# Performance work log

Hardware: AMD Instinct MI355X
Metric: run time of the kernel (lower is better)

The kernel has to match this reference:

```python
import jax, jax.numpy as jnp
import numpy as np

B, T, D = 256, 256, 96   # batch, seq (== block_size), d_model
H, E = 6, 16             # n_head, d_head = d_model // n_head
DFF = 4 * D              # feedforward hidden = 384
NOISE_STD = 0.1
EPS = 1e-5               # torch LayerNorm default eps


def setup_inputs() -> dict:
    key = jax.random.key(0)
    ks = jax.random.split(key, 10)
    s = 0.02
    return {
        "x":     jax.random.normal(ks[0], (B, T, D), jnp.float32),
        # per-head Q/K/V projections stacked: [H, D, E] (no bias, as in Head)
        "Wq":    jax.random.normal(ks[1], (H, D, E), jnp.float32) * s,
        "Wk":    jax.random.normal(ks[2], (H, D, E), jnp.float32) * s,
        "Wv":    jax.random.normal(ks[3], (H, D, E), jnp.float32) * s,
        "Wp":    jax.random.normal(ks[4], (D, D), jnp.float32) * s,
        "bp":    jnp.zeros((D,), jnp.float32),
        "ln1_g": jnp.ones((D,), jnp.float32),
        "ln1_b": jnp.zeros((D,), jnp.float32),
        "ln2_g": jnp.ones((D,), jnp.float32),
        "ln2_b": jnp.zeros((D,), jnp.float32),
        "W1":    jax.random.normal(ks[5], (D, DFF), jnp.float32) * s,
        "b1":    jnp.zeros((DFF,), jnp.float32),
        "W2":    jax.random.normal(ks[6], (DFF, D), jnp.float32) * s,
        "b2":    jnp.zeros((D,), jnp.float32),
    }


def layernorm(x, g, b):
    m = jnp.mean(x, axis=-1, keepdims=True)
    v = jnp.var(x, axis=-1, keepdims=True)
    return (x - m) * jax.lax.rsqrt(v + EPS) * g + b


def reference(x, Wq, Wk, Wv, Wp, bp, ln1_g, ln1_b, ln2_g, ln2_b, W1, b1, W2, b2):
    Bx, Tx, Dx = x.shape
    nk1, nk2 = jax.random.split(jax.random.key(42), 2)

    # --- self-attention branch (pre-norm) ---
    h = layernorm(x, ln1_g, ln1_b)
    q = jnp.einsum('btd,hde->bhte', h, Wq)
    k = jnp.einsum('btd,hde->bhte', h, Wk)
    v = jnp.einsum('btd,hde->bhte', h, Wv)
    scores = jnp.einsum('bhte,bhse->bhts', q, k) * (E ** -0.5)
    causal = jnp.tril(jnp.ones((Tx, Tx), bool))
    scores = jnp.where(causal, scores, -jnp.inf)
    a = jax.nn.softmax(scores, axis=-1)      # dropout = identity (eval)
    o = jnp.einsum('bhts,bhse->bhte', a, v)
    o = o.transpose(0, 2, 1, 3).reshape(Bx, Tx, Dx)  # concat heads
    o = o @ Wp + bp
    x = x + o + jax.random.normal(nk1, x.shape, x.dtype) * NOISE_STD

    # --- feedforward branch (pre-norm) ---
    h = layernorm(x, ln2_g, ln2_b)
    f = jax.nn.relu(h @ W1 + b1) @ W2 + b2   # dropout = identity (eval)
    x = x + f + jax.random.normal(nk2, x.shape, x.dtype) * NOISE_STD
    return x
```

## Files before the change

### kernel.cpp

```cpp
#include <hip/hip_runtime.h>
#include <hip/hip_bf16.h>
#include <stdint.h>


#define B_    256
#define T_    256
#define D_    96
#define H_    6
#define E_    16
#define DFF_  384
#define BT_   (B_*T_)
#define NTOK_ (BT_*D_)
#define WPN_  (96*96)
#define W1N_  (96*384)
#define W2N_  (384*96)
#define WTOT_ (WPN_+W1N_+W2N_)

typedef __hip_bfloat16 bf16;
typedef __attribute__((ext_vector_type(8))) short v8s;
typedef __attribute__((ext_vector_type(4))) float v4f;

__device__ __forceinline__ void wfence(){ __asm__ volatile("" ::: "memory"); }

__host__ __device__ inline uint32_t rotl32(uint32_t x, int r){ return (x<<r)|(x>>(32-r)); }

__host__ __device__ inline void tf2x32(uint32_t k0, uint32_t k1, uint32_t& x0, uint32_t& x1){
  uint32_t ks2 = k0 ^ k1 ^ 0x1BD11BDAu;
  x0 += k0; x1 += k1;
#define TF_R(r) { x0 += x1; x1 = rotl32(x1, r); x1 ^= x0; }
  TF_R(13) TF_R(15) TF_R(26) TF_R(6)
  x0 += k1;  x1 += ks2 + 1u;
  TF_R(17) TF_R(29) TF_R(16) TF_R(24)
  x0 += ks2; x1 += k0 + 2u;
  TF_R(13) TF_R(15) TF_R(26) TF_R(6)
  x0 += k0;  x1 += k1 + 3u;
  TF_R(17) TF_R(29) TF_R(16) TF_R(24)
  x0 += k1;  x1 += ks2 + 4u;
  TF_R(13) TF_R(15) TF_R(26) TF_R(6)
  x0 += ks2; x1 += k0 + 5u;
#undef TF_R
}

__device__ __forceinline__ float erfinv32(float x){
  float w = -0.69314718056f * __log2f((1.0f - x) * (1.0f + x));
  float p;
  if (w < 5.0f) {
    w -= 2.5f;
    p = 2.81022636e-08f;
    p = fmaf(p, w, 3.43273939e-07f);
    p = fmaf(p, w, -3.5233877e-06f);
    p = fmaf(p, w, -4.39150654e-06f);
    p = fmaf(p, w, 0.00021858087f);
    p = fmaf(p, w, -0.00125372503f);
    p = fmaf(p, w, -0.00417768164f);
    p = fmaf(p, w, 0.246640727f);
    p = fmaf(p, w, 1.50140941f);
  } else {
    w = sqrtf(w) - 3.0f;
    p = -0.000200214257f;
    p = fmaf(p, w, 0.000100950558f);
    p = fmaf(p, w, 0.00134934322f);
    p = fmaf(p, w, -0.00367342844f);
    p = fmaf(p, w, 0.00573950773f);
    p = fmaf(p, w, -0.0076224613f);
    p = fmaf(p, w, 0.00943887047f);
    p = fmaf(p, w, 1.00167406f);
    p = fmaf(p, w, 2.83297682f);
  }
  return p * x;
}

__device__ __forceinline__ float jax_normal(uint32_t k0, uint32_t k1, uint32_t j){
  uint32_t x0 = 0u, x1 = j;
  tf2x32(k0, k1, x0, x1);
  uint32_t bits = x0 ^ x1;
  float f = __uint_as_float((bits >> 9) | 0x3F800000u) - 1.0f;
  const float lo = -0.99999994f;
  float u = fmaxf(lo, fmaf(f, 2.0f, lo));
  return 1.41421356f * erfinv32(u);
}

__device__ __forceinline__ float blo(uint32_t u){ return __uint_as_float(u << 16); }
__device__ __forceinline__ float bhi(uint32_t u){ return __uint_as_float(u & 0xFFFF0000u); }
__device__ __forceinline__ uint16_t f2b(float f){
  union { bf16 h; uint16_t u; } x; x.h = __float2bfloat16(f); return x.u;
}
__device__ __forceinline__ uint32_t packbf(float a, float b){
  return (uint32_t)f2b(a) | ((uint32_t)f2b(b) << 16);
}

__global__ __launch_bounds__(256, 3)
void k_attn_fused(const float* __restrict__ x,
                  const float* __restrict__ Wq, const float* __restrict__ Wk,
                  const float* __restrict__ Wv,
                  const float* __restrict__ g1, const float* __restrict__ bln1,
                  bf16* __restrict__ o_ws,
                  const float* __restrict__ Wp, const float* __restrict__ W1,
                  const float* __restrict__ W2, bf16* __restrict__ wbuf)
{
  __shared__ __align__(16) uint16_t hts[64*104];
  __shared__ __align__(16) uint32_t wpl[48][52];
  __shared__ __align__(16) uint16_t Ks[256][24];
  __shared__ __align__(16) uint16_t Vt[16][264];

  const int tid  = threadIdx.x;
  const int bh   = blockIdx.x;
  const int b    = bh / H_, h = bh % H_;
  const int w    = tid >> 6;
  const int lane = tid & 63;
  const int quad = lane >> 4;
  const int l15  = lane & 15;

  if (tid < 54) {
    int id = bh*54 + tid;
    const float* src; bf16* dst; int k, n, N;
    if (id < WPN_)             { src = Wp; dst = wbuf;               k = id/96; n = id%96; N = 96; }
    else if (id < WPN_ + W1N_) { int t = id - WPN_;
                                 src = W1; dst = wbuf + WPN_;        k = t/384; n = t%384; N = 384; }
    else                       { int t = id - WPN_ - W1N_;
                                 src = W2; dst = wbuf + WPN_ + W1N_; k = t/96;  n = t%96;  N = 96; }
    int idx = ((k>>3)*(N>>4) + (n>>4))*128 + ((n&15)<<3) + (k&7);
    dst[idx] = __float2bfloat16(src[(size_t)k*N + n]);
  }

  for (int idx = tid; idx < 48*48; idx += 256) {
    int c = idx / 48, dp = idx % 48;
    int mat = c >> 4, e = c & 15;
    const float* Wm = (mat == 0 ? Wk : (mat == 1 ? Wv : Wq)) + h*(D_*E_);
    wpl[c][dp] = packbf(Wm[(2*dp)*16 + e], Wm[(2*dp+1)*16 + e]);
  }

  v4f qacc[4];
  {
    const int r  = lane >> 2;
    const int cg = lane & 3;
    float gv[24], bv[24];
    #pragma unroll
    for (int i = 0; i < 24; ++i) { gv[i] = g1[cg*24 + i]; bv[i] = bln1[cg*24 + i]; }

    for (int rt = 0; rt < 4; ++rt) {
      __syncthreads();
      const int lrow = w*16 + r;
      const int row  = rt*64 + lrow;
      const float4* xp = (const float4*)(x + ((size_t)(b*256 + row)*96 + cg*24));
      float xv[24];
      #pragma unroll
      for (int p = 0; p < 6; ++p) {
        float4 t4 = xp[p];
        xv[4*p+0] = t4.x; xv[4*p+1] = t4.y; xv[4*p+2] = t4.z; xv[4*p+3] = t4.w;
      }
      float s1 = 0.f, s2 = 0.f;
      #pragma unroll
      for (int i = 0; i < 24; ++i) { s1 += xv[i]; s2 = fmaf(xv[i], xv[i], s2); }
      s1 += __shfl_xor(s1, 1); s2 += __shfl_xor(s2, 1);
      s1 += __shfl_xor(s1, 2); s2 += __shfl_xor(s2, 2);
      float mm = s1 * (1.0f/96.0f);
      float rs = rsqrtf(s2 * (1.0f/96.0f) - mm*mm + 1e-5f);
      #pragma unroll
      for (int p = 0; p < 12; ++p) {
        float h0 = (xv[2*p]   - mm)*rs*gv[2*p]   + bv[2*p];
        float h1 = (xv[2*p+1] - mm)*rs*gv[2*p+1] + bv[2*p+1];
        *(uint32_t*)&hts[lrow*104 + cg*24 + 2*p] = packbf(h0, h1);
      }
      __syncthreads();

      v8s ah[3];
      #pragma unroll
      for (int ks = 0; ks < 3; ++ks)
        ah[ks] = *(const v8s*)&hts[(w*16 + l15)*104 + ks*32 + quad*8];
      #pragma unroll
      for (int nt = 0; nt < 3; ++nt) {
        v4f acc = {0.f,0.f,0.f,0.f};
        #pragma unroll
        for (int ks = 0; ks < 3; ++ks) {
          v8s bb = *(const v8s*)&wpl[nt*16 + l15][ks*16 + quad*4];
          acc = __builtin_amdgcn_mfma_f32_16x16x32_bf16(ah[ks], bb, acc, 0, 0, 0);
        }
        int tr0 = rt*64 + w*16 + quad*4;
        if (nt == 0) {
          #pragma unroll
          for (int r2 = 0; r2 < 4; ++r2) Ks[tr0 + r2][l15] = f2b(acc[r2]);
        } else if (nt == 1) {
          *(uint32_t*)&Vt[l15][tr0]     = packbf(acc[0], acc[1]);
          *(uint32_t*)&Vt[l15][tr0 + 2] = packbf(acc[2], acc[3]);
        } else {
          qacc[rt] = acc;
        }
      }
    }
  }
  __syncthreads();

  uint16_t* Pb = &hts[(w*16)*104];
  v8s qf[4];
  v8s zero8;
  #pragma unroll
  for (int j = 0; j < 8; ++j) zero8[j] = 0;
  #pragma unroll
  for (int rt = 0; rt < 4; ++rt) {
    wfence();
    #pragma unroll
    for (int r2 = 0; r2 < 4; ++r2)
      Pb[(quad*4 + r2)*40 + l15] = f2b(qacc[rt][r2] * 0.25f);
    wfence();
    qf[rt] = (quad < 2) ? *(const v8s*)&Pb[l15*40 + quad*8] : zero8;
  }

  v8s ones;
  #pragma unroll
  for (int j = 0; j < 8; ++j) ones[j] = (short)0x3F80;

  v4f oacc[4], lac[4];
  #pragma unroll
  for (int i = 0; i < 4; ++i) { oacc[i] = (v4f){0.f,0.f,0.f,0.f}; lac[i] = (v4f){0.f,0.f,0.f,0.f}; }

  for (int sb = 0; sb < 8; ++sb) {
    v8s kf0 = (quad < 2) ? *(const v8s*)&Ks[sb*32      + l15][quad*8] : zero8;
    v8s kf1 = (quad < 2) ? *(const v8s*)&Ks[sb*32 + 16 + l15][quad*8] : zero8;
    v8s vf  = *(const v8s*)&Vt[l15][sb*32 + quad*8];
    #pragma unroll
    for (int i = 0; i < 4; ++i) {
      int mt = 4*i + w;
      if (mt >= 2*sb) {
        v4f z = {0.f,0.f,0.f,0.f};
        v4f s0 = __builtin_amdgcn_mfma_f32_16x16x32_bf16(qf[i], kf0, z, 0, 0, 0);
        v4f s1 = __builtin_amdgcn_mfma_f32_16x16x32_bf16(qf[i], kf1, z, 0, 0, 0);
        const int qb  = mt*16 + quad*4;
        const int sc0 = sb*32 + l15, sc1 = sc0 + 16;
        wfence();
        #pragma unroll
        for (int r2 = 0; r2 < 4; ++r2) {
          float p0 = (sc0 > qb + r2) ? 0.f : __expf(s0[r2]);
          float p1 = (sc1 > qb + r2) ? 0.f : __expf(s1[r2]);
          Pb[(quad*4 + r2)*40 + l15]      = f2b(p0);
          Pb[(quad*4 + r2)*40 + 16 + l15] = f2b(p1);
        }
        wfence();
        v8s pf = *(const v8s*)&Pb[l15*40 + quad*8];
        oacc[i] = __builtin_amdgcn_mfma_f32_16x16x32_bf16(pf, vf,   oacc[i], 0, 0, 0);
        lac[i]  = __builtin_amdgcn_mfma_f32_16x16x32_bf16(pf, ones, lac[i],  0, 0, 0);
      }
    }
  }

  #pragma unroll
  for (int i = 0; i < 4; ++i) {
    int mt = 4*i + w;
    #pragma unroll
    for (int r2 = 0; r2 < 4; ++r2) {
      float inv = 1.0f / lac[i][r2];
      size_t idx = ((size_t)b*256 + mt*16 + quad*4 + r2)*96 + h*16 + l15;
      o_ws[idx] = __float2bfloat16(oacc[i][r2] * inv);
    }
  }
}

__global__ __launch_bounds__(256, 4)
void k_proj_ff(const float* __restrict__ x, const bf16* __restrict__ o_ws,
               const bf16* __restrict__ wb,
               const float* __restrict__ bp,
               const float* __restrict__ g2, const float* __restrict__ bln2,
               const float* __restrict__ b1, const float* __restrict__ b2,
               float* __restrict__ out,
               uint32_t n1k0, uint32_t n1k1, uint32_t n2k0, uint32_t n2k1)
{
  __shared__ __align__(16) uint16_t t2 [2][64][104];

  const bf16* wpb = wb;
  const bf16* w1b = wb + WPN_;
  const bf16* w2b = wb + WPN_ + W1N_;

  const int tid  = threadIdx.x;
  const int w    = tid >> 6;
  const int lane = tid & 63;
  const int quad = lane >> 4;
  const int l15  = lane & 15;
  const int rowbase = blockIdx.x * 64;
  const uint32_t jbase = (uint32_t)rowbase * 96u;

  #define BFRAG(Wb, Ndiv16, nt, k8) \
    (*(const v8s*)((Wb) + (((k8)*(Ndiv16) + (nt))*128 + l15*8)))

  float ff[24];
  {
    v8s ao[3];
    #pragma unroll
    for (int ks = 0; ks < 3; ++ks)
      ao[ks] = *(const v8s*)(o_ws + (size_t)(rowbase + w*16 + l15)*96 + ks*32 + quad*8);
    #pragma unroll
    for (int nt = 0; nt < 6; ++nt) {
      int col = nt*16 + l15;
      v4f acc = {0.f,0.f,0.f,0.f};
      #pragma unroll
      for (int ks = 0; ks < 3; ++ks)
        acc = __builtin_amdgcn_mfma_f32_16x16x32_bf16(ao[ks], BFRAG(wpb, 6, nt, ks*4+quad), acc, 0, 0, 0);
      float bpv = bp[col];
      #pragma unroll
      for (int r = 0; r < 4; ++r) {
        int row = w*16 + quad*4 + r;
        uint32_t j = jbase + (uint32_t)row*96u + (uint32_t)col;
        ff[nt*4+r] = acc[r] + bpv + x[j] + 0.1f * jax_normal(n1k0, n1k1, j);
      }
    }
  }

  {
    float mmv[4], rsv[4];
    #pragma unroll
    for (int r = 0; r < 4; ++r) {
      float s1 = 0.f, s2 = 0.f;
      #pragma unroll
      for (int nt = 0; nt < 6; ++nt) { float v = ff[nt*4+r]; s1 += v; s2 = fmaf(v, v, s2); }
      s1 += __shfl_xor(s1, 1); s2 += __shfl_xor(s2, 1);
      s1 += __shfl_xor(s1, 2); s2 += __shfl_xor(s2, 2);
      s1 += __shfl_xor(s1, 4); s2 += __shfl_xor(s2, 4);
      s1 += __shfl_xor(s1, 8); s2 += __shfl_xor(s2, 8);
      float mm = s1 * (1.0f/96.0f);
      mmv[r] = mm;
      rsv[r] = rsqrtf(s2 * (1.0f/96.0f) - mm*mm + 1e-5f);
    }
    float g2v[6], b2l[6];
    #pragma unroll
    for (int nt = 0; nt < 6; ++nt) { g2v[nt] = g2[nt*16 + l15]; b2l[nt] = bln2[nt*16 + l15]; }
    #pragma unroll
    for (int nt = 0; nt < 6; ++nt)
      #pragma unroll
      for (int r = 0; r < 4; ++r)
        t2[0][w*16 + quad*4 + r][nt*16 + l15] =
            f2b((ff[nt*4+r] - mmv[r]) * rsv[r] * g2v[nt] + b2l[nt]);
  }
  wfence();

  v8s ah[3];
  #pragma unroll
  for (int ks = 0; ks < 3; ++ks)
    ah[ks] = *(const v8s*)&t2[0][w*16 + l15][ks*32 + quad*8];
  v4f acc2[6];
  #pragma unroll
  for (int nt = 0; nt < 6; ++nt) acc2[nt] = (v4f){0.f,0.f,0.f,0.f};
  float n2v[24];

  #define FF1C(C, DST) { \
    _Pragma("unroll") \
    for (int nt = 0; nt < 6; ++nt) { \
      v4f a = {0.f,0.f,0.f,0.f}; \
      _Pragma("unroll") \
      for (int ks = 0; ks < 3; ++ks) \
        a = __builtin_amdgcn_mfma_f32_16x16x32_bf16(ah[ks], BFRAG(w1b, 24, (C)*6+nt, ks*4+quad), a, 0, 0, 0); \
      float b1v = b1[(C)*96 + nt*16 + l15]; \
      _Pragma("unroll") \
      for (int r = 0; r < 4; ++r) \
        DST[w*16 + quad*4 + r][nt*16 + l15] = f2b(fmaxf(a[r] + b1v, 0.f)); \
    } }

  #define FF2C(C, SRC) { \
    v8s af[3]; \
    _Pragma("unroll") \
    for (int ks = 0; ks < 3; ++ks) \
      af[ks] = *(const v8s*)&SRC[w*16 + l15][ks*32 + quad*8]; \
    _Pragma("unroll") \
    for (int nt = 0; nt < 6; ++nt) { \
      _Pragma("unroll") \
      for (int ks = 0; ks < 3; ++ks) \
        acc2[nt] = __builtin_amdgcn_mfma_f32_16x16x32_bf16(af[ks], BFRAG(w2b, 6, nt, ((C)*3+ks)*4+quad), acc2[nt], 0, 0, 0); \
    } }

  #define GEN6(C) { \
    _Pragma("unroll") \
    for (int i = 0; i < 6; ++i) { \
      int vv = (C)*6 + i; int nt2 = vv >> 2; int r2 = vv & 3; \
      int row = w*16 + quad*4 + r2; \
      uint32_t j = jbase + (uint32_t)row*96u + (uint32_t)(nt2*16 + l15); \
      n2v[vv] = jax_normal(n2k0, n2k1, j); \
    } }

  FF1C(0, t2[1])
  wfence();
  FF1C(1, t2[0])
  FF2C(0, t2[1])
  GEN6(0)
  wfence();
  FF1C(2, t2[1])
  FF2C(1, t2[0])
  GEN6(1)
  wfence();
  FF1C(3, t2[0])
  FF2C(2, t2[1])
  GEN6(2)
  wfence();
  FF2C(3, t2[0])
  GEN6(3)

  #pragma unroll
  for (int nt = 0; nt < 6; ++nt) {
    int col = nt*16 + l15;
    float b2v = b2[col];
    #pragma unroll
    for (int r = 0; r < 4; ++r) {
      int row = w*16 + quad*4 + r;
      out[(size_t)(rowbase + row)*96 + col] =
          ff[nt*4+r] + acc2[nt][r] + b2v + 0.1f * n2v[nt*4 + r];
    }
  }
  #undef GEN6
  #undef FF2C
  #undef FF1C
  #undef BFRAG
}

__global__ __launch_bounds__(256)
void k_zero(float* __restrict__ out)
{
  int i = blockIdx.x*256 + threadIdx.x;
  if (i < NTOK_) out[i] = 0.0f;
}

extern "C" void kernel_launch(void* const* d_in, const int* in_sizes, int n_in,
                              void* d_out, int out_size, void* d_ws, size_t ws_size,
                              hipStream_t stream) {
  const float* x    = (const float*)d_in[0];
  const float* Wq   = (const float*)d_in[1];
  const float* Wk   = (const float*)d_in[2];
  const float* Wv   = (const float*)d_in[3];
  const float* Wp   = (const float*)d_in[4];
  const float* bp   = (const float*)d_in[5];
  const float* g1   = (const float*)d_in[6];
  const float* bln1 = (const float*)d_in[7];
  const float* g2   = (const float*)d_in[8];
  const float* bln2 = (const float*)d_in[9];
  const float* W1   = (const float*)d_in[10];
  const float* b1   = (const float*)d_in[11];
  const float* W2   = (const float*)d_in[12];
  const float* b2   = (const float*)d_in[13];
  float* out = (float*)d_out;

  size_t need = (size_t)NTOK_*sizeof(bf16) + (size_t)WTOT_*sizeof(bf16);
  if (ws_size < need) {
    hipLaunchKernelGGL(k_zero, dim3((NTOK_ + 255)/256), dim3(256), 0, stream, out);
    return;
  }
  bf16* o_ws = (bf16*)d_ws;
  bf16* wbuf = o_ws + NTOK_;

  uint32_t n1k0 = 0u, n1k1 = 0u; tf2x32(0u, 42u, n1k0, n1k1);
  uint32_t n2k0 = 0u, n2k1 = 1u; tf2x32(0u, 42u, n2k0, n2k1);

  hipLaunchKernelGGL(k_attn_fused, dim3(B_*H_), dim3(256), 0, stream,
                     x, Wq, Wk, Wv, g1, bln1, o_ws, Wp, W1, W2, wbuf);
  hipLaunchKernelGGL(k_proj_ff, dim3(BT_/64), dim3(256), 0, stream,
                     x, o_ws, wbuf, bp, g2, bln2, b1, b2, out,
                     n1k0, n1k1, n2k0, n2k1);
}
```

Baseline: 197.3 us.

## Split proj/FF row tiles across wave pairs to halve per-wave work and registers

```diff
diff --git a/kernel.cpp b/kernel.cpp
--- a/kernel.cpp
+++ b/kernel.cpp
@@ -255,7 +255,7 @@
   }
 }
 
-__global__ __launch_bounds__(256, 4)
+__global__ __launch_bounds__(256, 8)
 void k_proj_ff(const float* __restrict__ x, const bf16* __restrict__ o_ws,
                const bf16* __restrict__ wb,
                const float* __restrict__ bp,
@@ -264,7 +264,8 @@
                float* __restrict__ out,
                uint32_t n1k0, uint32_t n1k1, uint32_t n2k0, uint32_t n2k1)
 {
-  __shared__ __align__(16) uint16_t t2 [2][64][104];
+  __shared__ __align__(16) uint16_t t2[2][32][104];
+  __shared__ __align__(8)  float2  st[32][2];
 
   const bf16* wpb = wb;
   const bf16* w1b = wb + WPN_;
@@ -272,23 +273,27 @@
 
   const int tid  = threadIdx.x;
   const int w    = tid >> 6;
+  const int wp   = w >> 1;
+  const int s    = w & 1;
   const int lane = tid & 63;
   const int quad = lane >> 4;
   const int l15  = lane & 15;
-  const int rowbase = blockIdx.x * 64;
+  const int rowbase = blockIdx.x * 32;
   const uint32_t jbase = (uint32_t)rowbase * 96u;
+  const int rloc = wp*16 + quad*4;
 
   #define BFRAG(Wb, Ndiv16, nt, k8) \
     (*(const v8s*)((Wb) + (((k8)*(Ndiv16) + (nt))*128 + l15*8)))
 
-  float ff[24];
+  float ff[12];
   {
     v8s ao[3];
     #pragma unroll
     for (int ks = 0; ks < 3; ++ks)
-      ao[ks] = *(const v8s*)(o_ws + (size_t)(rowbase + w*16 + l15)*96 + ks*32 + quad*8);
-    #pragma unroll
-    for (int nt = 0; nt < 6; ++nt) {
+      ao[ks] = *(const v8s*)(o_ws + (size_t)(rowbase + wp*16 + l15)*96 + ks*32 + quad*8);
+    #pragma unroll
+    for (int nt3 = 0; nt3 < 3; ++nt3) {
+      int nt = s*3 + nt3;
       int col = nt*16 + l15;
       v4f acc = {0.f,0.f,0.f,0.f};
       #pragma unroll
@@ -297,112 +302,124 @@
       float bpv = bp[col];
       #pragma unroll
       for (int r = 0; r < 4; ++r) {
-        int row = w*16 + quad*4 + r;
+        int row = rloc + r;
         uint32_t j = jbase + (uint32_t)row*96u + (uint32_t)col;
-        ff[nt*4+r] = acc[r] + bpv + x[j] + 0.1f * jax_normal(n1k0, n1k1, j);
+        ff[nt3*4+r] = acc[r] + bpv + x[j] + 0.1f * jax_normal(n1k0, n1k1, j);
       }
     }
   }
 
   {
-    float mmv[4], rsv[4];
+    float s1p[4], s2p[4];
     #pragma unroll
     for (int r = 0; r < 4; ++r) {
       float s1 = 0.f, s2 = 0.f;
       #pragma unroll
-      for (int nt = 0; nt < 6; ++nt) { float v = ff[nt*4+r]; s1 += v; s2 = fmaf(v, v, s2); }
+      for (int nt3 = 0; nt3 < 3; ++nt3) { float v = ff[nt3*4+r]; s1 += v; s2 = fmaf(v, v, s2); }
       s1 += __shfl_xor(s1, 1); s2 += __shfl_xor(s2, 1);
       s1 += __shfl_xor(s1, 2); s2 += __shfl_xor(s2, 2);
       s1 += __shfl_xor(s1, 4); s2 += __shfl_xor(s2, 4);
       s1 += __shfl_xor(s1, 8); s2 += __shfl_xor(s2, 8);
+      s1p[r] = s1; s2p[r] = s2;
+    }
+    if (l15 == 0) {
+      #pragma unroll
+      for (int r = 0; r < 4; ++r) st[rloc + r][s] = make_float2(s1p[r], s2p[r]);
+    }
+    __syncthreads();
+
+    float g2v[3], b2l[3];
+    #pragma unroll
+    for (int nt3 = 0; nt3 < 3; ++nt3) {
+      g2v[nt3] = g2[s*48 + nt3*16 + l15];
+      b2l[nt3] = bln2[s*48 + nt3*16 + l15];
+    }
+    #pragma unroll
+    for (int r = 0; r < 4; ++r) {
+      float2 pa = st[rloc + r][0], pb = st[rloc + r][1];
+      float s1 = pa.x + pb.x, s2 = pa.y + pb.y;
       float mm = s1 * (1.0f/96.0f);
-      mmv[r] = mm;
-      rsv[r] = rsqrtf(s2 * (1.0f/96.0f) - mm*mm + 1e-5f);
-    }
-    float g2v[6], b2l[6];
-    #pragma unroll
-    for (int nt = 0; nt < 6; ++nt) { g2v[nt] = g2[nt*16 + l15]; b2l[nt] = bln2[nt*16 + l15]; }
-    #pragma unroll
-    for (int nt = 0; nt < 6; ++nt)
-      #pragma unroll
-      for (int r = 0; r < 4; ++r)
-        t2[0][w*16 + quad*4 + r][nt*16 + l15] =
-            f2b((ff[nt*4+r] - mmv[r]) * rsv[r] * g2v[nt] + b2l[nt]);
-  }
-  wfence();
+      float rs = rsqrtf(s2 * (1.0f/96.0f) - mm*mm + 1e-5f);
+      #pragma unroll
+      for (int nt3 = 0; nt3 < 3; ++nt3)
+        t2[0][rloc + r][s*48 + nt3*16 + l15] =
+            f2b((ff[nt3*4+r] - mm) * rs * g2v[nt3] + b2l[nt3]);
+    }
+  }
+  __syncthreads();
 
   v8s ah[3];
   #pragma unroll
   for (int ks = 0; ks < 3; ++ks)
-    ah[ks] = *(const v8s*)&t2[0][w*16 + l15][ks*32 + quad*8];
-  v4f acc2[6];
-  #pragma unroll
-  for (int nt = 0; nt < 6; ++nt) acc2[nt] = (v4f){0.f,0.f,0.f,0.f};
-  float n2v[24];
+    ah[ks] = *(const v8s*)&t2[0][wp*16 + l15][ks*32 + quad*8];
+  v4f acc2[3];
+  #pragma unroll
+  for (int nt3 = 0; nt3 < 3; ++nt3) acc2[nt3] = (v4f){0.f,0.f,0.f,0.f};
+  float n2v[12];
 
   #define FF1C(C, DST) { \
     _Pragma("unroll") \
-    for (int nt = 0; nt < 6; ++nt) { \
+    for (int nt3 = 0; nt3 < 3; ++nt3) { \
       v4f a = {0.f,0.f,0.f,0.f}; \
       _Pragma("unroll") \
       for (int ks = 0; ks < 3; ++ks) \
-        a = __builtin_amdgcn_mfma_f32_16x16x32_bf16(ah[ks], BFRAG(w1b, 24, (C)*6+nt, ks*4+quad), a, 0, 0, 0); \
-      float b1v = b1[(C)*96 + nt*16 + l15]; \
+        a = __builtin_amdgcn_mfma_f32_16x16x32_bf16(ah[ks], BFRAG(w1b, 24, (C)*6 + s*3 + nt3, ks*4+quad), a, 0, 0, 0); \
+      float b1v = b1[(C)*96 + s*48 + nt3*16 + l15]; \
       _Pragma("unroll") \
       for (int r = 0; r < 4; ++r) \
-        DST[w*16 + quad*4 + r][nt*16 + l15] = f2b(fmaxf(a[r] + b1v, 0.f)); \
+        DST[rloc + r][s*48 + nt3*16 + l15] = f2b(fmaxf(a[r] + b1v, 0.f)); \
     } }
 
   #define FF2C(C, SRC) { \
     v8s af[3]; \
     _Pragma("unroll") \
     for (int ks = 0; ks < 3; ++ks) \
-      af[ks] = *(const v8s*)&SRC[w*16 + l15][ks*32 + quad*8]; \
+      af[ks] = *(const v8s*)&SRC[wp*16 + l15][ks*32 + quad*8]; \
     _Pragma("unroll") \
-    for (int nt = 0; nt < 6; ++nt) { \
+    for (int nt3 = 0; nt3 < 3; ++nt3) { \
       _Pragma("unroll") \
       for (int ks = 0; ks < 3; ++ks) \
-        acc2[nt] = __builtin_amdgcn_mfma_f32_16x16x32_bf16(af[ks], BFRAG(w2b, 6, nt, ((C)*3+ks)*4+quad), acc2[nt], 0, 0, 0); \
+        acc2[nt3] = __builtin_amdgcn_mfma_f32_16x16x32_bf16(af[ks], BFRAG(w2b, 6, s*3 + nt3, ((C)*3+ks)*4+quad), acc2[nt3], 0, 0, 0); \
     } }
 
-  #define GEN6(C) { \
+  #define GEN3(C) { \
     _Pragma("unroll") \
-    for (int i = 0; i < 6; ++i) { \
-      int vv = (C)*6 + i; int nt2 = vv >> 2; int r2 = vv & 3; \
-      int row = w*16 + quad*4 + r2; \
-      uint32_t j = jbase + (uint32_t)row*96u + (uint32_t)(nt2*16 + l15); \
+    for (int i = 0; i < 3; ++i) { \
+      int vv = (C)*3 + i; int nt2 = vv >> 2; int r2 = vv & 3; \
+      int row = rloc + r2; \
+      uint32_t j = jbase + (uint32_t)row*96u + (uint32_t)(s*48 + nt2*16 + l15); \
       n2v[vv] = jax_normal(n2k0, n2k1, j); \
     } }
 
   FF1C(0, t2[1])
-  wfence();
+  __syncthreads();
   FF1C(1, t2[0])
   FF2C(0, t2[1])
-  GEN6(0)
-  wfence();
+  GEN3(0)
+  __syncthreads();
   FF1C(2, t2[1])
   FF2C(1, t2[0])
-  GEN6(1)
-  wfence();
+  GEN3(1)
+  __syncthreads();
   FF1C(3, t2[0])
   FF2C(2, t2[1])
-  GEN6(2)
-  wfence();
+  GEN3(2)
+  __syncthreads();
   FF2C(3, t2[0])
-  GEN6(3)
-
-  #pragma unroll
-  for (int nt = 0; nt < 6; ++nt) {
-    int col = nt*16 + l15;
+  GEN3(3)
+
+  #pragma unroll
+  for (int nt3 = 0; nt3 < 3; ++nt3) {
+    int col = s*48 + nt3*16 + l15;
     float b2v = b2[col];
     #pragma unroll
     for (int r = 0; r < 4; ++r) {
-      int row = w*16 + quad*4 + r;
+      int row = rloc + r;
       out[(size_t)(rowbase + row)*96 + col] =
-          ff[nt*4+r] + acc2[nt][r] + b2v + 0.1f * n2v[nt*4 + r];
-    }
-  }
-  #undef GEN6
+          ff[nt3*4+r] + acc2[nt3][r] + b2v + 0.1f * n2v[nt3*4 + r];
+    }
+  }
+  #undef GEN3
   #undef FF2C
   #undef FF1C
   #undef BFRAG
@@ -447,7 +464,7 @@
 
   hipLaunchKernelGGL(k_attn_fused, dim3(B_*H_), dim3(256), 0, stream,
                      x, Wq, Wk, Wv, g1, bln1, o_ws, Wp, W1, W2, wbuf);
-  hipLaunchKernelGGL(k_proj_ff, dim3(BT_/64), dim3(256), 0, stream,
+  hipLaunchKernelGGL(k_proj_ff, dim3(BT_/32), dim3(256), 0, stream,
                      x, o_ws, wbuf, bp, g2, bln2, b1, b2, out,
                      n1k0, n1k1, n2k0, n2k1);
 }
```

New measurement: 205.3 us. 1.04x slower.
